# Optimization experiments

Hardware: AMD Instinct MI355X
Metric: run time of the kernel (lower is better)

The kernel has to match this reference:

```python
import jax, jax.numpy as jnp
import numpy as np

H = 16          # attention_head_num
DH = 64         # attention_head_size
D = H * DH      # out_dim / model dim
SIZE_PER_HEAD = 64  # scaling denominator (init arg, used as sqrt divisor)


def setup_inputs() -> dict:
    key = jax.random.key(0)
    ks = jax.random.split(key, 12)
    B, S = 2, 2048
    scale = 1.0 / np.sqrt(D)
    inp = {
        "qx": jax.random.normal(ks[0], (B, S, D), dtype=jnp.float32),
        "kx": jax.random.normal(ks[1], (B, S, D), dtype=jnp.float32),
        "vx": jax.random.normal(ks[2], (B, S, D), dtype=jnp.float32),
        "Wq": jax.random.normal(ks[3], (D, D), dtype=jnp.float32) * scale,
        "bq": jnp.zeros((D,), dtype=jnp.float32),
        "Wk": jax.random.normal(ks[4], (D, D), dtype=jnp.float32) * scale,
        "bk": jnp.zeros((D,), dtype=jnp.float32),
        "Wv": jax.random.normal(ks[5], (D, D), dtype=jnp.float32) * scale,
        "bv": jnp.zeros((D,), dtype=jnp.float32),
        "Wo": jax.random.normal(ks[6], (D, D), dtype=jnp.float32) * scale,
        "bo": jnp.zeros((D,), dtype=jnp.float32),
    }
    return inp


def reference(qx, kx, vx, Wq, bq, Wk, bk, Wv, bv, Wo, bo):
    B, Sq, _ = qx.shape
    Sk = kx.shape[1]
    # QKV projections
    q = qx @ Wq + bq  # [B,Sq,D]
    k = kx @ Wk + bk  # [B,Sk,D]
    v = vx @ Wv + bv  # [B,Sk,D]
    # split heads -> [B,H,S,DH]
    q = q.reshape(B, Sq, H, DH).transpose(0, 2, 1, 3)
    k = k.reshape(B, Sk, H, DH).transpose(0, 2, 1, 3)
    v = v.reshape(B, Sk, H, DH).transpose(0, 2, 1, 3)
    # scores [B,H,Sq,Sk]; NOTE: original divides by sqrt(size_per_head)
    scores = jnp.einsum("bhqd,bhkd->bhqk", q, k) / jnp.sqrt(
        jnp.asarray(SIZE_PER_HEAD, dtype=q.dtype)
    )
    probs = jax.nn.softmax(scores, axis=-1)
    ctx = jnp.einsum("bhqk,bhkd->bhqd", probs, v)  # [B,H,Sq,DH]
    ctx = ctx.transpose(0, 2, 1, 3).reshape(B, Sq, D)
    return ctx @ Wo + bo
```

## Files before the change

kernel.cpp:

```cpp
#include <hip/hip_runtime.h>

typedef _Float16 half_t;
typedef _Float16 half8 __attribute__((ext_vector_type(8)));
typedef __fp16 fp16x2 __attribute__((ext_vector_type(2)));
typedef float f32x16 __attribute__((ext_vector_type(16)));
typedef float f32x4v __attribute__((ext_vector_type(4)));
typedef unsigned uint2v __attribute__((ext_vector_type(2)));

#define MFMA32(A, B, C) __builtin_amdgcn_mfma_f32_32x32x16_f16(A, B, C, 0, 0, 0)

#if __has_builtin(__builtin_amdgcn_exp2f)
#define EXP2F(x) __builtin_amdgcn_exp2f(x)
#else
#define EXP2F(x) exp2f(x)
#endif

static constexpr int S = 2048;
static constexpr int D = 1024;
static constexpr float QSCALE = 0.18033688011112042f;


__device__ __forceinline__ void gload_lds16(const void* g, void* l) {
    __builtin_amdgcn_global_load_lds(
        (const __attribute__((address_space(1))) unsigned int*)g,
        (__attribute__((address_space(3))) unsigned int*)l, 16, 0, 0);
}

__global__ __launch_bounds__(256) void cvtw(
    const float* __restrict__ x0, const float* __restrict__ x1, const float* __restrict__ x2,
    const float* __restrict__ w0, const float* __restrict__ w1,
    const float* __restrict__ w2, const float* __restrict__ w3,
    half_t* __restrict__ o0, half_t* __restrict__ o1, half_t* __restrict__ o2,
    half_t* __restrict__ wt)
{
    __shared__ char sm[33280];
    int y = blockIdx.y;
    int t = threadIdx.x;
    if (y < 3) {
        float (*tile)[65] = (float(*)[65])sm;
        const float* src = (y == 0) ? x0 : (y == 1) ? x1 : x2;
        half_t* dst = (y == 0) ? o0 : (y == 1) ? o1 : o2;
        int mt = blockIdx.x >> 4, kt = blockIdx.x & 15;
        const float* sbase = src + (size_t)(mt * 128) * D + kt * 64;
        int rr = t >> 4, col = (t & 15) * 4;
#pragma unroll
        for (int p = 0; p < 8; ++p) {
            int row = rr + p * 16;
            f32x4v v = *(const f32x4v*)(sbase + (size_t)row * D + col);
            tile[row][col] = v[0]; tile[row][col + 1] = v[1];
            tile[row][col + 2] = v[2]; tile[row][col + 3] = v[3];
        }
        __syncthreads();
        int c = t >> 5, r0 = t & 31;
        half_t* dbase = dst + ((size_t)(mt * 16 + kt)) * 8192;
#pragma unroll
        for (int i = 0; i < 4; ++i) {
            int row = r0 + 32 * i;
            half8 h;
#pragma unroll
            for (int j = 0; j < 8; ++j) h[j] = (half_t)tile[row][c * 8 + j];
            *(half8*)(dbase + ((size_t)c * 128 + row) * 8) = h;
        }
    } else {
        float (*tile)[129] = (float(*)[129])sm;
        int w = blockIdx.x >> 7;
        const float* W = (w == 0) ? w0 : (w == 1) ? w1 : (w == 2) ? w2 : w3;
        int idx = blockIdx.x & 127;
        int nt = idx >> 4, kt = idx & 15;
        const float* sbase = W + (size_t)(kt * 64) * D + nt * 128;
        int kr = t >> 5, col = (t & 31) * 4;
#pragma unroll
        for (int p = 0; p < 8; ++p) {
            int k = kr + p * 8;
            f32x4v v = *(const f32x4v*)(sbase + (size_t)k * D + col);
            tile[k][col] = v[0]; tile[k][col + 1] = v[1];
            tile[k][col + 2] = v[2]; tile[k][col + 3] = v[3];
        }
        __syncthreads();
        int c = t >> 5, r0 = t & 31;
        half_t* dbase = wt + (size_t)w * 1048576 + ((size_t)(nt * 16 + kt)) * 8192;
#pragma unroll
        for (int i = 0; i < 4; ++i) {
            int n = r0 + 32 * i;
            half8 h;
#pragma unroll
            for (int j = 0; j < 8; ++j) h[j] = (half_t)tile[c * 8 + j][n];
            *(half8*)(dbase + ((size_t)c * 128 + n) * 8) = h;
        }
    }
}

__global__ __launch_bounds__(256, 4) void gemm_qkv(
    const half_t* __restrict__ a0, const half_t* __restrict__ a1, const half_t* __restrict__ a2,
    const half_t* __restrict__ wt,
    const float* __restrict__ b0, const float* __restrict__ b1, const float* __restrict__ b2,
    half_t* __restrict__ qh, half_t* __restrict__ kh, half_t* __restrict__ vt)
{
    __shared__ char smem[24576];
    half_t* As = (half_t*)smem;
    half_t* Bs = (half_t*)(smem + 16384);
    int z = blockIdx.z;
    const half_t* A = (z == 0) ? a0 : (z == 1) ? a1 : a2;
    const half_t* BT = wt + (size_t)z * 1048576;
    const float* bias = (z == 0) ? b0 : (z == 1) ? b1 : b2;
    int L = blockIdx.x;
    int w = L >> 3;
    int mt = (L & 7) * 4 + (w & 3);
    int nt64 = w >> 2;
    int ntS = nt64 >> 1, nh = nt64 & 1;
    int m0 = mt * 128, n0 = nt64 * 64;
    int tid = threadIdx.x, lane = tid & 63, wave = tid >> 6;
    int ml = lane & 31, hi = lane >> 5;
    int wm = (wave & 1) * 64, wn = (wave >> 1) * 32;

    f32x16 acc0 = {}, acc1 = {};

    for (int kt = 0; kt < 16; ++kt) {
        __syncthreads();
        const half_t* Aslab = A + ((size_t)(mt * 16 + kt)) * 8192;
        const half_t* Bslab = BT + ((size_t)(ntS * 16 + kt)) * 8192;
#pragma unroll
        for (int j = 0; j < 4; ++j) {
            int s = wave * 4 + j;
            gload_lds16(Aslab + s * 512 + lane * 8, As + s * 512);
        }
#pragma unroll
        for (int j = 0; j < 2; ++j) {
            int s2 = wave * 2 + j;
            gload_lds16(Bslab + ((size_t)s2 * 128 + nh * 64) * 8 + lane * 8, Bs + s2 * 512);
        }
        __syncthreads();
#pragma unroll
        for (int ks = 0; ks < 4; ++ks) {
            int co = 2 * ks + hi;
            half8 af0 = *(const half8*)(As + (size_t)(co * 128 + wm + ml) * 8);
            half8 af1 = *(const half8*)(As + (size_t)(co * 128 + wm + 32 + ml) * 8);
            half8 bf  = *(const half8*)(Bs + (size_t)(co * 64 + wn + ml) * 8);
            acc0 = MFMA32(af0, bf, acc0);
            acc1 = MFMA32(af1, bf, acc1);
        }
    }

    __syncthreads();
    half_t* buf = (half_t*)smem;
    {
        int nl = wn + ml;
        float bv = bias[n0 + nl];
        int c = (nl >> 3) & 7, j = nl & 7;
#pragma unroll
        for (int mt2 = 0; mt2 < 2; ++mt2) {
            f32x16 av = (mt2 == 0) ? acc0 : acc1;
#pragma unroll
            for (int r = 0; r < 16; ++r) {
                int rl = wm + mt2 * 32 + 4 * hi + (r & 3) + 8 * (r >> 2);
                float v = av[r] + bv;
                if (z == 0) v *= QSCALE;
                if (z <= 1) {
                    buf[((size_t)rl * 8 + (c ^ (rl & 7))) * 8 + j] = (half_t)v;
                } else {
                    int cc = rl >> 3, js = rl & 7;
                    buf[((size_t)nl * 16 + (cc ^ (nl & 7))) * 8 + js] = (half_t)v;
                }
            }
        }
    }
    __syncthreads();
    int bq_ = m0 >> 11, skt = (m0 >> 7) & 15, h0 = nt64;
    half_t* dstm = (z == 0) ? qh : (z == 1) ? kh : vt;
    half_t* gdst = dstm + ((size_t)(bq_ * 16 + h0)) * 131072 + (size_t)skt * 8192;
#pragma unroll
    for (int i = 0; i < 4; ++i) {
        int o = tid + 256 * i;
        half8 v8;
        int off;
        if (z <= 1) {
            int c = o >> 7, r = o & 127;
            v8 = *(const half8*)(buf + (((size_t)r * 8 + (c ^ (r & 7))) * 8));
            off = (c * 128 + r) * 8;
        } else {
            int cc = o >> 6, dd = o & 63;
            v8 = *(const half8*)(buf + (((size_t)dd * 16 + (cc ^ (dd & 7))) * 8));
            off = (cc * 64 + dd) * 8;
        }
        *(half8*)(gdst + off) = v8;
    }
}

__global__ __launch_bounds__(256, 4) void gemm_out(
    const half_t* __restrict__ A, const half_t* __restrict__ BT,
    const float* __restrict__ bias, float* __restrict__ out)
{
    __shared__ char smem[24576];
    half_t* As = (half_t*)smem;
    half_t* Bs = (half_t*)(smem + 16384);
    int L = blockIdx.x;
    int w = L >> 3;
    int mt = (L & 7) * 4 + (w & 3);
    int nt64 = w >> 2;
    int ntS = nt64 >> 1, nh = nt64 & 1;
    int m0 = mt * 128, n0 = nt64 * 64;
    int tid = threadIdx.x, lane = tid & 63, wave = tid >> 6;
    int ml = lane & 31, hi = lane >> 5;
    int wm = (wave & 1) * 64, wn = (wave >> 1) * 32;

    f32x16 acc0 = {}, acc1 = {};

    for (int kt = 0; kt < 16; ++kt) {
        __syncthreads();
        const half_t* Aslab = A + ((size_t)(mt * 16 + kt)) * 8192;
        const half_t* Bslab = BT + ((size_t)(ntS * 16 + kt)) * 8192;
#pragma unroll
        for (int j = 0; j < 4; ++j) {
            int s = wave * 4 + j;
            gload_lds16(Aslab + s * 512 + lane * 8, As + s * 512);
        }
#pragma unroll
        for (int j = 0; j < 2; ++j) {
            int s2 = wave * 2 + j;
            gload_lds16(Bslab + ((size_t)s2 * 128 + nh * 64) * 8 + lane * 8, Bs + s2 * 512);
        }
        __syncthreads();
#pragma unroll
        for (int ks = 0; ks < 4; ++ks) {
            int co = 2 * ks + hi;
            half8 af0 = *(const half8*)(As + (size_t)(co * 128 + wm + ml) * 8);
            half8 af1 = *(const half8*)(As + (size_t)(co * 128 + wm + 32 + ml) * 8);
            half8 bf  = *(const half8*)(Bs + (size_t)(co * 64 + wn + ml) * 8);
            acc0 = MFMA32(af0, bf, acc0);
            acc1 = MFMA32(af1, bf, acc1);
        }
    }

    int n = n0 + wn + ml;
    float bv = bias[n];
#pragma unroll
    for (int mt2 = 0; mt2 < 2; ++mt2) {
        f32x16 av = (mt2 == 0) ? acc0 : acc1;
        int rbase = m0 + wm + mt2 * 32 + 4 * hi;
#pragma unroll
        for (int r = 0; r < 16; ++r) {
            int row = rbase + (r & 3) + 8 * (r >> 2);
            out[(size_t)row * D + n] = av[r] + bv;
        }
    }
}

__global__ __launch_bounds__(512, 4) void attn(
    const half_t* __restrict__ qh, const half_t* __restrict__ kh,
    const half_t* __restrict__ vt, half_t* __restrict__ ctx)
{
    __shared__ char smem[49152];

    int L = blockIdx.x;
    int slot = L >> 3;
    int bh = (L & 7) + 8 * (slot >> 4);
    int sq = slot & 15;
    int b_ = bh >> 4, h = bh & 15;

    int tid = threadIdx.x, lane = tid & 63, wave = tid >> 6;
    int ml = lane & 31, hi = lane >> 5;
    int qq = wave & 3, th = wave >> 2;
    const half_t* qslab = qh + (size_t)bh * 131072 + (size_t)sq * 8192;
    const half_t* khead = kh + (size_t)bh * 131072;
    const half_t* vhead = vt + (size_t)bh * 131072;

    half_t* Vs = (half_t*)(smem + 32768);

    {
        half_t* QB = Vs;
        half_t* K0 = (half_t*)(smem);
#pragma unroll
        for (int j = 0; j < 2; ++j) {
            int s = wave * 2 + j;
            gload_lds16(qslab + s * 512 + lane * 8, QB + s * 512);
            gload_lds16(khead + s * 512 + lane * 8, K0 + s * 512);
        }
    }
    __syncthreads();
    half8 qf[4];
    {
        half_t* QB = Vs;
#pragma unroll
        for (int ks = 0; ks < 4; ++ks)
            qf[ks] = *(const half8*)(QB + ((size_t)((2 * ks + hi) * 128 + qq * 32 + ml)) * 8);
    }
    __syncthreads();

    f32x16 oacc[2] = {};
    float lsumA = 0.0f, lsumB = 0.0f;
    fp16x2 one2; one2.x = (__fp16)1.0f; one2.y = (__fp16)1.0f;
    const f32x16 sinit = {-10.0f, -10.0f, -10.0f, -10.0f, -10.0f, -10.0f, -10.0f, -10.0f,
                          -10.0f, -10.0f, -10.0f, -10.0f, -10.0f, -10.0f, -10.0f, -10.0f};

    int t0 = th * 2, t1 = th * 2 + 1;

    for (int it = 0; it < 16; ++it) {
        int bb = it & 1;
        {
            const half_t* vslab = vhead + (size_t)it * 8192;
#pragma unroll
            for (int j = 0; j < 2; ++j) {
                int s = wave * 2 + j;
                gload_lds16(vslab + s * 512 + lane * 8, Vs + s * 512);
            }
        }
        if (it < 15) {
            const half_t* kslab = khead + (size_t)(it + 1) * 8192;
            half_t* Kd = (half_t*)(smem + (bb ^ 1) * 16384);
#pragma unroll
            for (int j = 0; j < 2; ++j) {
                int s = wave * 2 + j;
                gload_lds16(kslab + s * 512 + lane * 8, Kd + s * 512);
            }
        }
        half_t* Ks = (half_t*)(smem + bb * 16384);

        f32x16 sv0 = sinit, sv1 = sinit;
        __builtin_amdgcn_s_setprio(1);
#pragma unroll
        for (int ks = 0; ks < 4; ++ks) {
            half8 kf0 = *(const half8*)(Ks + ((size_t)((2 * ks + hi) * 128 + t0 * 32 + ml)) * 8);
            half8 kf1 = *(const half8*)(Ks + ((size_t)((2 * ks + hi) * 128 + t1 * 32 + ml)) * 8);
            sv0 = MFMA32(kf0, qf[ks], sv0);
            sv1 = MFMA32(kf1, qf[ks], sv1);
        }
        __builtin_amdgcn_s_setprio(0);

        unsigned pkv0[8];
        {
            float lsA = lsumA;
#pragma unroll
            for (int j = 0; j < 8; ++j) {
                float pa = EXP2F(sv0[2 * j]);
                float pb = EXP2F(sv0[2 * j + 1]);
#if __has_builtin(__builtin_amdgcn_cvt_pkrtz)
                fp16x2 h2 = __builtin_amdgcn_cvt_pkrtz(pa, pb);
#else
                fp16x2 h2; h2.x = (__fp16)pa; h2.y = (__fp16)pb;
#endif
                pkv0[j] = __builtin_bit_cast(unsigned, h2);
#if __has_builtin(__builtin_amdgcn_fdot2)
                lsA = __builtin_amdgcn_fdot2(h2, one2, lsA, false);
#else
                lsA += pa + pb;
#endif
            }
            lsumA = lsA;
        }

        __syncthreads();

#pragma unroll
        for (int kp = 0; kp < 2; ++kp) {
            union { unsigned u[4]; half8 h; } fr;
#if __has_builtin(__builtin_amdgcn_permlane32_swap)
            uint2v w0 = __builtin_amdgcn_permlane32_swap(pkv0[4 * kp + 0], pkv0[4 * kp + 2], false, false);
            uint2v w1 = __builtin_amdgcn_permlane32_swap(pkv0[4 * kp + 1], pkv0[4 * kp + 3], false, false);
            fr.u[0] = w0.x; fr.u[1] = w1.x; fr.u[2] = w0.y; fr.u[3] = w1.y;
#else
            unsigned e0 = pkv0[4 * kp + 0], e1 = pkv0[4 * kp + 1];
            unsigned o0 = pkv0[4 * kp + 2], o1 = pkv0[4 * kp + 3];
            unsigned s0u = hi ? e0 : o0, s1u = hi ? e1 : o1;
            unsigned k0u = hi ? o0 : e0, k1u = hi ? o1 : e1;
            unsigned r0 = __shfl_xor(s0u, 32, 64);
            unsigned r1 = __shfl_xor(s1u, 32, 64);
            fr.u[0] = hi ? r0 : k0u; fr.u[1] = hi ? r1 : k1u;
            fr.u[2] = hi ? k0u : r0; fr.u[3] = hi ? k1u : r1;
#endif
            __builtin_amdgcn_s_setprio(1);
#pragma unroll
            for (int dt = 0; dt < 2; ++dt) {
                half8 vf = *(const half8*)(Vs + ((size_t)((4 * t0 + 2 * kp + hi) * 64 + dt * 32 + ml)) * 8);
                oacc[dt] = MFMA32(fr.h, vf, oacc[dt]);
            }
            __builtin_amdgcn_s_setprio(0);
        }

        unsigned pkv1[8];
        {
            float lsB = lsumB;
#pragma unroll
            for (int j = 0; j < 8; ++j) {
                float pa = EXP2F(sv1[2 * j]);
                float pb = EXP2F(sv1[2 * j + 1]);
#if __has_builtin(__builtin_amdgcn_cvt_pkrtz)
                fp16x2 h2 = __builtin_amdgcn_cvt_pkrtz(pa, pb);
#else
                fp16x2 h2; h2.x = (__fp16)pa; h2.y = (__fp16)pb;
#endif
                pkv1[j] = __builtin_bit_cast(unsigned, h2);
#if __has_builtin(__builtin_amdgcn_fdot2)
                lsB = __builtin_amdgcn_fdot2(h2, one2, lsB, false);
#else
                lsB += pa + pb;
#endif
            }
            lsumB = lsB;
        }

#pragma unroll
        for (int kp = 0; kp < 2; ++kp) {
            union { unsigned u[4]; half8 h; } fr;
#if __has_builtin(__builtin_amdgcn_permlane32_swap)
            uint2v w0 = __builtin_amdgcn_permlane32_swap(pkv1[4 * kp + 0], pkv1[4 * kp + 2], false, false);
            uint2v w1 = __builtin_amdgcn_permlane32_swap(pkv1[4 * kp + 1], pkv1[4 * kp + 3], false, false);
            fr.u[0] = w0.x; fr.u[1] = w1.x; fr.u[2] = w0.y; fr.u[3] = w1.y;
#else
            unsigned e0 = pkv1[4 * kp + 0], e1 = pkv1[4 * kp + 1];
            unsigned o0 = pkv1[4 * kp + 2], o1 = pkv1[4 * kp + 3];
            unsigned s0u = hi ? e0 : o0, s1u = hi ? e1 : o1;
            unsigned k0u = hi ? o0 : e0, k1u = hi ? o1 : e1;
            unsigned r0 = __shfl_xor(s0u, 32, 64);
            unsigned r1 = __shfl_xor(s1u, 32, 64);
            fr.u[0] = hi ? r0 : k0u; fr.u[1] = hi ? r1 : k1u;
            fr.u[2] = hi ? k0u : r0; fr.u[3] = hi ? k1u : r1;
#endif
            __builtin_amdgcn_s_setprio(1);
#pragma unroll
            for (int dt = 0; dt < 2; ++dt) {
                half8 vf = *(const half8*)(Vs + ((size_t)((4 * t1 + 2 * kp + hi) * 64 + dt * 32 + ml)) * 8);
                oacc[dt] = MFMA32(fr.h, vf, oacc[dt]);
            }
            __builtin_amdgcn_s_setprio(0);
        }

        __syncthreads();
    }

    float lsum = lsumA + lsumB;
    float lt = lsum + __shfl_xor(lsum, 32, 64);

    float* OB = (float*)(smem + (size_t)qq * 8192);
    if (th == 1) {
#pragma unroll
        for (int dt = 0; dt < 2; ++dt)
#pragma unroll
            for (int r = 0; r < 16; ++r) {
                int q = 4 * hi + (r & 3) + 8 * (r >> 2);
                OB[q * 64 + dt * 32 + ml] = oacc[dt][r];
            }
    }
    __syncthreads();
    if (th == 0) {
#pragma unroll
        for (int dt = 0; dt < 2; ++dt)
#pragma unroll
            for (int r = 0; r < 16; ++r) {
                int q = 4 * hi + (r & 3) + 8 * (r >> 2);
                oacc[dt][r] += OB[q * 64 + dt * 32 + ml];
            }
    }
    __syncthreads();
    float* Lbuf = (float*)(smem + 32768);
    if (th == 1 && hi == 0) Lbuf[qq * 32 + ml] = lt;
    __syncthreads();
    if (th == 0 && hi == 0) Lbuf[qq * 32 + ml] += lt;
    __syncthreads();
    if (th == 0) {
        half_t* cslab = ctx + ((size_t)((b_ * 16 + sq) * 16 + h)) * 8192;
#pragma unroll
        for (int dt = 0; dt < 2; ++dt)
#pragma unroll
            for (int r = 0; r < 16; ++r) {
                int qw = 4 * hi + (r & 3) + 8 * (r >> 2);
                int q = qq * 32 + qw;
                int d = dt * 32 + ml;
                float linv = __builtin_amdgcn_rcpf(Lbuf[q]);
                cslab[((d >> 3) * 128 + q) * 8 + (d & 7)] =
                    (half_t)(oacc[dt][r] * linv);
            }
    }
}

extern "C" void kernel_launch(void* const* d_in, const int* in_sizes, int n_in,
                              void* d_out, int out_size, void* d_ws, size_t ws_size,
                              hipStream_t stream)
{
    const float* qx = (const float*)d_in[0];
    const float* kx = (const float*)d_in[1];
    const float* vx = (const float*)d_in[2];
    const float* Wq = (const float*)d_in[3];
    const float* bq = (const float*)d_in[4];
    const float* Wk = (const float*)d_in[5];
    const float* bk = (const float*)d_in[6];
    const float* Wv = (const float*)d_in[7];
    const float* bv = (const float*)d_in[8];
    const float* Wo = (const float*)d_in[9];
    const float* bo = (const float*)d_in[10];
    float* out = (float*)d_out;

    half_t* ws = (half_t*)d_ws;
    const size_t NT = (size_t)4096 * 1024;
    half_t* qxh = ws;
    half_t* kxh = qxh + NT;
    half_t* vxh = kxh + NT;
    half_t* wt = vxh + NT;
    half_t* qh = wt + (size_t)4 * 1048576;
    half_t* kh = qh + NT;
    half_t* vtr = kh + NT;
    half_t* ctx = vtr + NT;

    cvtw<<<dim3(512, 4), 256, 0, stream>>>(qx, kx, vx, Wq, Wk, Wv, Wo, qxh, kxh, vxh, wt);
    gemm_qkv<<<dim3(512, 1, 3), 256, 0, stream>>>(qxh, kxh, vxh, wt, bq, bk, bv, qh, kh, vtr);
    attn<<<dim3(512, 1, 1), 512, 0, stream>>>(qh, kh, vtr, ctx);
    gemm_out<<<dim3(512, 1, 1), 256, 0, stream>>>(ctx, wt + (size_t)3 * 1048576, bo, out);
}
```

Baseline: 212.1 us.

## Split attention blocks to 64 queries with double-buffered K and V tiles

The attention kernel now runs 1024 blocks of 256 threads, each handling 64 query rows instead of 128, and iterates over 64-key tiles instead of 128. K and V are both double-buffered in a smaller 32KB LDS footprint, which removes the mid-iteration barrier that previously guarded the single V buffer. The intent is more blocks per CU and better overlap of loads with compute. The cost is that K and V are reloaded twice as often per query row, and each loop iteration does less work relative to its barrier.

```diff
diff --git a/kernel.cpp b/kernel.cpp
--- a/kernel.cpp
+++ b/kernel.cpp
@@ -245,44 +245,45 @@
     }
 }
 
-__global__ __launch_bounds__(512, 4) void attn(
+__global__ __launch_bounds__(256, 4) void attn(
     const half_t* __restrict__ qh, const half_t* __restrict__ kh,
     const half_t* __restrict__ vt, half_t* __restrict__ ctx)
 {
-    __shared__ char smem[49152];
+    __shared__ char smem[32768];
 
     int L = blockIdx.x;
     int slot = L >> 3;
-    int bh = (L & 7) + 8 * (slot >> 4);
-    int sq = slot & 15;
+    int bh = (L & 7) + 8 * (slot >> 5);
+    int sq = slot & 31;
     int b_ = bh >> 4, h = bh & 15;
+    int sq128 = sq >> 1, qhalf = sq & 1;
 
     int tid = threadIdx.x, lane = tid & 63, wave = tid >> 6;
     int ml = lane & 31, hi = lane >> 5;
-    int qq = wave & 3, th = wave >> 2;
-    const half_t* qslab = qh + (size_t)bh * 131072 + (size_t)sq * 8192;
+    int qq = wave & 1, th = wave >> 1;
+    const half_t* qslab = qh + (size_t)bh * 131072 + (size_t)sq128 * 8192;
     const half_t* khead = kh + (size_t)bh * 131072;
     const half_t* vhead = vt + (size_t)bh * 131072;
 
-    half_t* Vs = (half_t*)(smem + 32768);
-
     {
-        half_t* QB = Vs;
+        half_t* QB = (half_t*)(smem + 16384);
         half_t* K0 = (half_t*)(smem);
+        half_t* V0 = (half_t*)(smem + 8192);
 #pragma unroll
         for (int j = 0; j < 2; ++j) {
             int s = wave * 2 + j;
-            gload_lds16(qslab + s * 512 + lane * 8, QB + s * 512);
-            gload_lds16(khead + s * 512 + lane * 8, K0 + s * 512);
+            gload_lds16(qslab + ((size_t)(s * 128 + 64 * qhalf)) * 8 + lane * 8, QB + s * 512);
+            gload_lds16(khead + ((size_t)(s * 128)) * 8 + lane * 8, K0 + s * 512);
+            gload_lds16(vhead + ((size_t)(s * 64)) * 8 + lane * 8, V0 + s * 512);
         }
     }
     __syncthreads();
     half8 qf[4];
     {
-        half_t* QB = Vs;
+        half_t* QB = (half_t*)(smem + 16384);
 #pragma unroll
         for (int ks = 0; ks < 4; ++ks)
-            qf[ks] = *(const half8*)(QB + ((size_t)((2 * ks + hi) * 128 + qq * 32 + ml)) * 8);
+            qf[ks] = *(const half8*)(QB + ((size_t)((2 * ks + hi) * 64 + qq * 32 + ml)) * 8);
     }
     __syncthreads();
 
@@ -292,74 +293,68 @@
     const f32x16 sinit = {-10.0f, -10.0f, -10.0f, -10.0f, -10.0f, -10.0f, -10.0f, -10.0f,
                           -10.0f, -10.0f, -10.0f, -10.0f, -10.0f, -10.0f, -10.0f, -10.0f};
 
-    int t0 = th * 2, t1 = th * 2 + 1;
-
-    for (int it = 0; it < 16; ++it) {
+    for (int it = 0; it < 32; ++it) {
         int bb = it & 1;
-        {
-            const half_t* vslab = vhead + (size_t)it * 8192;
+        if (it < 31) {
+            int nx = it + 1;
+            const half_t* kslab = khead + (size_t)(nx >> 1) * 8192;
+            const half_t* vslab = vhead + (size_t)(nx >> 1) * 8192;
+            int rh = (nx & 1) * 64;
+            int ch = (nx & 1) * 8;
+            half_t* Kd = (half_t*)(smem + (bb ^ 1) * 16384);
+            half_t* Vd = (half_t*)(smem + 8192 + (bb ^ 1) * 16384);
 #pragma unroll
             for (int j = 0; j < 2; ++j) {
                 int s = wave * 2 + j;
-                gload_lds16(vslab + s * 512 + lane * 8, Vs + s * 512);
-            }
-        }
-        if (it < 15) {
-            const half_t* kslab = khead + (size_t)(it + 1) * 8192;
-            half_t* Kd = (half_t*)(smem + (bb ^ 1) * 16384);
-#pragma unroll
-            for (int j = 0; j < 2; ++j) {
-                int s = wave * 2 + j;
-                gload_lds16(kslab + s * 512 + lane * 8, Kd + s * 512);
+                gload_lds16(kslab + ((size_t)(s * 128 + rh)) * 8 + lane * 8, Kd + s * 512);
+                gload_lds16(vslab + ((size_t)((ch + s) * 64)) * 8 + lane * 8, Vd + s * 512);
             }
         }
         half_t* Ks = (half_t*)(smem + bb * 16384);
-
-        f32x16 sv0 = sinit, sv1 = sinit;
+        half_t* Vs = (half_t*)(smem + 8192 + bb * 16384);
+
+        f32x16 sv = sinit;
         __builtin_amdgcn_s_setprio(1);
 #pragma unroll
         for (int ks = 0; ks < 4; ++ks) {
-            half8 kf0 = *(const half8*)(Ks + ((size_t)((2 * ks + hi) * 128 + t0 * 32 + ml)) * 8);
-            half8 kf1 = *(const half8*)(Ks + ((size_t)((2 * ks + hi) * 128 + t1 * 32 + ml)) * 8);
-            sv0 = MFMA32(kf0, qf[ks], sv0);
-            sv1 = MFMA32(kf1, qf[ks], sv1);
+            half8 kf = *(const half8*)(Ks + ((size_t)((2 * ks + hi) * 64 + th * 32 + ml)) * 8);
+            sv = MFMA32(kf, qf[ks], sv);
         }
         __builtin_amdgcn_s_setprio(0);
 
-        unsigned pkv0[8];
+        unsigned pkv[8];
         {
-            float lsA = lsumA;
+            float lsA = lsumA, lsB = lsumB;
 #pragma unroll
             for (int j = 0; j < 8; ++j) {
-                float pa = EXP2F(sv0[2 * j]);
-                float pb = EXP2F(sv0[2 * j + 1]);
+                float pa = EXP2F(sv[2 * j]);
+                float pb = EXP2F(sv[2 * j + 1]);
 #if __has_builtin(__builtin_amdgcn_cvt_pkrtz)
                 fp16x2 h2 = __builtin_amdgcn_cvt_pkrtz(pa, pb);
 #else
                 fp16x2 h2; h2.x = (__fp16)pa; h2.y = (__fp16)pb;
 #endif
-                pkv0[j] = __builtin_bit_cast(unsigned, h2);
+                pkv[j] = __builtin_bit_cast(unsigned, h2);
 #if __has_builtin(__builtin_amdgcn_fdot2)
-                lsA = __builtin_amdgcn_fdot2(h2, one2, lsA, false);
+                if (j & 1) lsB = __builtin_amdgcn_fdot2(h2, one2, lsB, false);
+                else       lsA = __builtin_amdgcn_fdot2(h2, one2, lsA, false);
 #else
-                lsA += pa + pb;
+                if (j & 1) lsB += pa + pb; else lsA += pa + pb;
 #endif
             }
-            lsumA = lsA;
-        }
-
-        __syncthreads();
+            lsumA = lsA; lsumB = lsB;
+        }
 
 #pragma unroll
         for (int kp = 0; kp < 2; ++kp) {
             union { unsigned u[4]; half8 h; } fr;
 #if __has_builtin(__builtin_amdgcn_permlane32_swap)
-            uint2v w0 = __builtin_amdgcn_permlane32_swap(pkv0[4 * kp + 0], pkv0[4 * kp + 2], false, false);
-            uint2v w1 = __builtin_amdgcn_permlane32_swap(pkv0[4 * kp + 1], pkv0[4 * kp + 3], false, false);
+            uint2v w0 = __builtin_amdgcn_permlane32_swap(pkv[4 * kp + 0], pkv[4 * kp + 2], false, false);
+            uint2v w1 = __builtin_amdgcn_permlane32_swap(pkv[4 * kp + 1], pkv[4 * kp + 3], false, false);
             fr.u[0] = w0.x; fr.u[1] = w1.x; fr.u[2] = w0.y; fr.u[3] = w1.y;
 #else
-            unsigned e0 = pkv0[4 * kp + 0], e1 = pkv0[4 * kp + 1];
-            unsigned o0 = pkv0[4 * kp + 2], o1 = pkv0[4 * kp + 3];
+            unsigned e0 = pkv[4 * kp + 0], e1 = pkv[4 * kp + 1];
+            unsigned o0 = pkv[4 * kp + 2], o1 = pkv[4 * kp + 3];
             unsigned s0u = hi ? e0 : o0, s1u = hi ? e1 : o1;
             unsigned k0u = hi ? o0 : e0, k1u = hi ? o1 : e1;
             unsigned r0 = __shfl_xor(s0u, 32, 64);
@@ -370,55 +365,7 @@
             __builtin_amdgcn_s_setprio(1);
 #pragma unroll
             for (int dt = 0; dt < 2; ++dt) {
-                half8 vf = *(const half8*)(Vs + ((size_t)((4 * t0 + 2 * kp + hi) * 64 + dt * 32 + ml)) * 8);
-                oacc[dt] = MFMA32(fr.h, vf, oacc[dt]);
-            }
-            __builtin_amdgcn_s_setprio(0);
-        }
-
-        unsigned pkv1[8];
-        {
-            float lsB = lsumB;
-#pragma unroll
-            for (int j = 0; j < 8; ++j) {
-                float pa = EXP2F(sv1[2 * j]);
-                float pb = EXP2F(sv1[2 * j + 1]);
-#if __has_builtin(__builtin_amdgcn_cvt_pkrtz)
-                fp16x2 h2 = __builtin_amdgcn_cvt_pkrtz(pa, pb);
-#else
-                fp16x2 h2; h2.x = (__fp16)pa; h2.y = (__fp16)pb;
-#endif
-                pkv1[j] = __builtin_bit_cast(unsigned, h2);
-#if __has_builtin(__builtin_amdgcn_fdot2)
-                lsB = __builtin_amdgcn_fdot2(h2, one2, lsB, false);
-#else
-                lsB += pa + pb;
-#endif
-            }
-            lsumB = lsB;
-        }
-
-#pragma unroll
-        for (int kp = 0; kp < 2; ++kp) {
-            union { unsigned u[4]; half8 h; } fr;
-#if __has_builtin(__builtin_amdgcn_permlane32_swap)
-            uint2v w0 = __builtin_amdgcn_permlane32_swap(pkv1[4 * kp + 0], pkv1[4 * kp + 2], false, false);
-            uint2v w1 = __builtin_amdgcn_permlane32_swap(pkv1[4 * kp + 1], pkv1[4 * kp + 3], false, false);
-            fr.u[0] = w0.x; fr.u[1] = w1.x; fr.u[2] = w0.y; fr.u[3] = w1.y;
-#else
-            unsigned e0 = pkv1[4 * kp + 0], e1 = pkv1[4 * kp + 1];
-            unsigned o0 = pkv1[4 * kp + 2], o1 = pkv1[4 * kp + 3];
-            unsigned s0u = hi ? e0 : o0, s1u = hi ? e1 : o1;
-            unsigned k0u = hi ? o0 : e0, k1u = hi ? o1 : e1;
-            unsigned r0 = __shfl_xor(s0u, 32, 64);
-            unsigned r1 = __shfl_xor(s1u, 32, 64);
-            fr.u[0] = hi ? r0 : k0u; fr.u[1] = hi ? r1 : k1u;
-            fr.u[2] = hi ? k0u : r0; fr.u[3] = hi ? k1u : r1;
-#endif
-            __builtin_amdgcn_s_setprio(1);
-#pragma unroll
-            for (int dt = 0; dt < 2; ++dt) {
-                half8 vf = *(const half8*)(Vs + ((size_t)((4 * t1 + 2 * kp + hi) * 64 + dt * 32 + ml)) * 8);
+                half8 vf = *(const half8*)(Vs + ((size_t)((th * 4 + 2 * kp + hi) * 64 + dt * 32 + ml)) * 8);
                 oacc[dt] = MFMA32(fr.h, vf, oacc[dt]);
             }
             __builtin_amdgcn_s_setprio(0);
@@ -451,22 +398,23 @@
             }
     }
     __syncthreads();
-    float* Lbuf = (float*)(smem + 32768);
+    float* Lbuf = (float*)(smem + 16384);
     if (th == 1 && hi == 0) Lbuf[qq * 32 + ml] = lt;
     __syncthreads();
     if (th == 0 && hi == 0) Lbuf[qq * 32 + ml] += lt;
     __syncthreads();
     if (th == 0) {
-        half_t* cslab = ctx + ((size_t)((b_ * 16 + sq) * 16 + h)) * 8192;
+        half_t* cslab = ctx + ((size_t)((b_ * 16 + sq128) * 16 + h)) * 8192;
 #pragma unroll
         for (int dt = 0; dt < 2; ++dt)
 #pragma unroll
             for (int r = 0; r < 16; ++r) {
                 int qw = 4 * hi + (r & 3) + 8 * (r >> 2);
                 int q = qq * 32 + qw;
+                int rq = qhalf * 64 + q;
                 int d = dt * 32 + ml;
                 float linv = __builtin_amdgcn_rcpf(Lbuf[q]);
-                cslab[((d >> 3) * 128 + q) * 8 + (d & 7)] =
+                cslab[((d >> 3) * 128 + rq) * 8 + (d & 7)] =
                     (half_t)(oacc[dt][r] * linv);
             }
     }
@@ -502,6 +450,6 @@
 
     cvtw<<<dim3(512, 4), 256, 0, stream>>>(qx, kx, vx, Wq, Wk, Wv, Wo, qxh, kxh, vxh, wt);
     gemm_qkv<<<dim3(512, 1, 3), 256, 0, stream>>>(qxh, kxh, vxh, wt, bq, bk, bv, qh, kh, vtr);
-    attn<<<dim3(512, 1, 1), 512, 0, stream>>>(qh, kh, vtr, ctx);
+    attn<<<dim3(1024, 1, 1), 256, 0, stream>>>(qh, kh, vtr, ctx);
     gemm_out<<<dim3(512, 1, 1), 256, 0, stream>>>(ctx, wt + (size_t)3 * 1048576, bo, out);
 }
```

After: 219.4 us. +3.4%, slower.
